# Kernel optimization log

Hardware: AMD Instinct MI355X
Metric: run time of the kernel (lower is better)

The kernel has to match this reference:

```python
import jax, jax.numpy as jnp
import numpy as np

B, T, D = 16, 512, 256          # batch, seq_len, d_model (= num features = num graph nodes N)
H, MC, K, DE, DH = 4, 4, 3, 10, 128
GS, SS, AS = 4, 6, 4            # global/sector/asset regime states
TAU = 0.5
STEPS = 3                       # diffusion steps
HID = max(64, D)
DEC_H = max(64, D // 2)


def setup_inputs() -> dict:
    key = jax.random.key(0)
    ks = iter(jax.random.split(key, 64))

    def nrm(shape, s=0.02):
        return (s * jax.random.normal(next(ks), shape)).astype(jnp.float32)

    z = lambda *s: jnp.zeros(s, jnp.float32)
    o = lambda *s: jnp.ones(s, jnp.float32)
    p = dict(
        x=jax.random.normal(next(ks), (B, T, D), dtype=jnp.float32),
        # hierarchical regime controller
        gW1=nrm((D, HID)), gb1=z(HID), g_ln_w=o(HID), g_ln_b=z(HID),
        gW2=nrm((HID, GS)), gb2=z(GS),
        sW1=nrm((D, HID)), sb1=z(HID), sW2=nrm((HID, D * SS)), sb2=z(D * SS),
        aW1=nrm((D, HID)), ab1=z(HID), aW2=nrm((HID, D * AS)), ab2=z(D * AS),
        global_prior=z(GS), sector_prior=z(SS), asset_prior=z(AS),
        g2f=nrm((GS, D)),
        sector_emb=jax.random.normal(next(ks), (SS, D), dtype=jnp.float32),
        asset_emb=jax.random.normal(next(ks), (AS, D), dtype=jnp.float32),
        # bidirectional temporal scan (BI-Mamba stand-in)
        decay_f=nrm((D,), 1.0), decay_b=nrm((D,), 1.0),
        tW=nrm((D, D)), tb=z(D),
        # Bayesian MAGAC + diffusion graph prior
        psi=nrm((H, D, DE), 0.1), log_sigma=jnp.full((H,), -2.0, jnp.float32),
        step_logits=jnp.linspace(-1.0, 0.5, STEPS).astype(jnp.float32),
        noise_scale=jnp.full((STEPS,), 0.05, jnp.float32),
        Wk=nrm((K + 1, T, DH)),
        mean_w=nrm((DH,)), mean_b=z(), lv_w=nrm((DH,)), lv_b=z(),
        # risk-aware decoder
        dW1=nrm((D, DEC_H)), db1=z(DEC_H), d_ln_w=o(DEC_H), d_ln_b=z(DEC_H),
        mW=nrm((DEC_H,)), mb=z(), lvW=nrm((DEC_H,)), lvb=z(),
        cW=nrm((DEC_H,)), cb=z(),
    )
    return p


def _ln(h, w, b):
    m = h.mean(-1, keepdims=True)
    v = h.var(-1, keepdims=True)  # biased, matches torch LayerNorm
    return (h - m) / jnp.sqrt(v + 1e-5) * w + b


def _gelu(h):
    return jax.nn.gelu(h, approximate=False)


def _gumbel_softmax(k, logits):
    u = jax.random.uniform(k, logits.shape, minval=1e-6, maxval=1.0 - 1e-6)
    g = -jnp.log(-jnp.log(u))
    return jax.nn.softmax((logits + g) / TAU, axis=-1)


def _fwd(x, gW1, gb1, g_ln_w, g_ln_b, gW2, gb2, sW1, sb1, sW2, sb2,
         aW1, ab1, aW2, ab2, global_prior, sector_prior, asset_prior,
         g2f, sector_emb, asset_emb, decay_f, decay_b, tW, tb,
         psi, log_sigma, step_logits, noise_scale, Wk,
         mean_w, mean_b, lv_w, lv_b,
         dW1, db1, d_ln_w, d_ln_b, mW, mb, lvW, lvb, cW, cb):
    rk = jax.random.key(42)
    k_g, k_s, k_a, k_eps, k_diff = jax.random.split(rk, 5)

    # ---- hierarchical regime controller ----
    seq_mean = x.mean(1)                               # (B, D)
    diff_summary = (x[:, 1:] - x[:, :-1]).mean(1)      # (B, D)
    g_logits = _gelu(_ln(seq_mean @ gW1 + gb1, g_ln_w, g_ln_b)) @ gW2 + gb2
    s_logits = (_gelu(seq_mean @ sW1 + sb1) @ sW2 + sb2).reshape(B, D, SS)
    a_logits = (_gelu(diff_summary @ aW1 + ab1) @ aW2 + ab2).reshape(B, D, AS)
    g_probs = _gumbel_softmax(k_g, g_logits)
    s_probs = _gumbel_softmax(k_s, s_logits)
    a_probs = _gumbel_softmax(k_a, a_logits)
    global_gate = g_probs @ g2f                                   # (B, D)
    # diagonal of einsum('bfs,sd->bfd') == einsum('bfs,sf->bf')
    sector_gate = jnp.einsum('bfs,sf->bf', s_probs, sector_emb)
    asset_gate = jnp.einsum('bfs,sf->bf', a_probs, asset_emb)
    feature_gate = jax.nn.sigmoid(global_gate + sector_gate + asset_gate)
    gated_x = x * feature_gate[:, None, :]

    # ---- bidirectional temporal EMA scan (BI-Mamba stand-in) ----
    af = jax.nn.sigmoid(decay_f)
    abk = jax.nn.sigmoid(decay_b)
    xs = gated_x.transpose(1, 0, 2)                    # (T, B, D)

    def ema(a):
        def step(h, xt):
            h = a * h + (1.0 - a) * xt
            return h, h
        return step

    _, hf = jax.lax.scan(ema(af), jnp.zeros_like(xs[0]), xs)
    _, hb = jax.lax.scan(ema(abk), jnp.zeros_like(xs[0]), xs[::-1])
    temporal = (hf + hb[::-1]).transpose(1, 0, 2) @ tW + tb       # (B, T, D)
    node_major = temporal.transpose(0, 2, 1)                      # (B, N=D, T)

    # ---- Bayesian adjacency sampling (MC samples per head) ----
    logits = jnp.einsum('hne,hme->hnm', psi, psi) / jnp.sqrt(jnp.float32(DE))
    sigma = jnp.exp(log_sigma)                                    # (H,)
    eps = jax.random.normal(k_eps, (MC, H, D, D))
    A = jax.nn.softmax(logits[None] + sigma[None, :, None, None] * eps, axis=-1)

    # ---- diffusion refinement guided by regime features ----
    ctx = feature_gate.mean(0)
    ctx = ctx / (jnp.linalg.norm(ctx) + 1e-6)
    outer = ctx[:, None] * ctx[None, :]
    outer = outer / jnp.maximum(outer.sum(-1, keepdims=True), 1e-6)
    dkeys = jax.random.split(k_diff, STEPS)
    for s in range(STEPS):                             # fixed small loop, vectorized over (MC,H)
        alpha = jax.nn.sigmoid(step_logits[s])
        noise = noise_scale[s] * jax.random.normal(dkeys[s], A.shape)
        A = alpha * A + (1.0 - alpha) * outer + noise
        A = 0.5 * (A + jnp.swapaxes(A, -1, -2))
        A = jax.nn.softmax(A, axis=-1)

    # ---- K-hop graph conv, averaged over MC samples and heads ----
    Z = jnp.einsum('bnt,td->bnd', node_major, Wk[0])[None, None]  # hop 0
    P = jnp.broadcast_to(node_major, (MC, H, B, D, T))
    for k in range(1, K + 1):
        P = jnp.einsum('mhnp,mhbpt->mhbnt', A, P)
        Z = Z + jnp.einsum('mhbnt,td->mhbnd', P, Wk[k])
    Z = Z.mean((0, 1))                                            # (B, N, DH)
    graph_mean = Z @ mean_w + mean_b                              # (B, N)
    graph_logvar = Z @ lv_w + lv_b                                # (B, N)

    # ---- risk-aware decoder ----
    feat = _ln(_gelu(graph_mean @ dW1 + db1), d_ln_w, d_ln_b)     # (B, DEC_H)
    mean = feat @ mW + mb
    dec_logvar = feat @ lvW + lvb
    _cvar = jax.nn.sigmoid(feat @ cW + cb)  # auxiliary head (not in returned output)
    var = jnp.exp(dec_logvar) + jnp.exp(graph_logvar).sum(1)
    log_var = jnp.log(var)
    return jnp.stack([mean, log_var], axis=-1)                    # (B, 2)


def reference(x, gW1, gb1, g_ln_w, g_ln_b, gW2, gb2, sW1, sb1, sW2, sb2,
              aW1, ab1, aW2, ab2, global_prior, sector_prior, asset_prior,
              g2f, sector_emb, asset_emb, decay_f, decay_b, tW, tb,
              psi, log_sigma, step_logits, noise_scale, Wk,
              mean_w, mean_b, lv_w, lv_b,
              dW1, db1, d_ln_w, d_ln_b, mW, mb, lvW, lvb, cW, cb):
    return _fwd(x, gW1, gb1, g_ln_w, g_ln_b, gW2, gb2, sW1, sb1, sW2, sb2,
                aW1, ab1, aW2, ab2, global_prior, sector_prior, asset_prior,
                g2f, sector_emb, asset_emb, decay_f, decay_b, tW, tb,
                psi, log_sigma, step_logits, noise_scale, Wk,
                mean_w, mean_b, lv_w, lv_b,
                dW1, db1, d_ln_w, d_ln_b, mW, mb, lvW, lvb, cW, cb)
```

## Files before the change

### kernel.cpp

```cpp
#include <hip/hip_runtime.h>
#include <stdint.h>

#define PARTITIONABLE 1

namespace {

struct TFPair { uint32_t a, b; };

__host__ __device__ constexpr uint32_t rotl32(uint32_t x, int d) {
  return (x << d) | (x >> (32 - d));
}

__host__ __device__ constexpr TFPair tf2x32(uint32_t k0, uint32_t k1,
                                            uint32_t x0, uint32_t x1) {
  uint32_t k2 = k0 ^ k1 ^ 0x1BD11BDAu;
  x0 += k0; x1 += k1;
  x0 += x1; x1 = rotl32(x1, 13); x1 ^= x0;
  x0 += x1; x1 = rotl32(x1, 15); x1 ^= x0;
  x0 += x1; x1 = rotl32(x1, 26); x1 ^= x0;
  x0 += x1; x1 = rotl32(x1, 6);  x1 ^= x0;
  x0 += k1; x1 += k2 + 1u;
  x0 += x1; x1 = rotl32(x1, 17); x1 ^= x0;
  x0 += x1; x1 = rotl32(x1, 29); x1 ^= x0;
  x0 += x1; x1 = rotl32(x1, 16); x1 ^= x0;
// ... 71 lines not shown
__device__ __forceinline__ float erfinv_f32(float x) {
  float w = -log1pf(-x * x);
  float p;
  if (w < 5.0f) {
    w -= 2.5f;
    p = 2.81022636e-08f;
    p = fmaf(p, w, 3.43273939e-07f);
    p = fmaf(p, w, -3.5233877e-06f);
    p = fmaf(p, w, -4.39150654e-06f);
    p = fmaf(p, w, 0.00021858087f);
    p = fmaf(p, w, -0.00125372503f);
    p = fmaf(p, w, -0.00417768164f);
    p = fmaf(p, w, 0.246640727f);
    p = fmaf(p, w, 1.50140941f);
  } else {
    w = sqrtf(w) - 3.0f;
    p = -0.000200214257f;
    p = fmaf(p, w, 0.000100950558f);
    p = fmaf(p, w, 0.00134934322f);
    p = fmaf(p, w, -0.00367342844f);
    p = fmaf(p, w, 0.00573950773f);
    p = fmaf(p, w, -0.0076224613f);
    p = fmaf(p, w, 0.00943887047f);
    p = fmaf(p, w, 1.00167406f);
    p = fmaf(p, w, 2.83297682f);
  }
  return p * x;
}

__device__ __forceinline__ float normal_from(uint32_t k0, uint32_t k1,
                                             uint32_t idx, uint32_t half) {
  const float lo = -0x1.fffffep-1f;
  float f = bits_to_u01(rbits(k0, k1, idx, half));
  float u = fmaxf(lo, f * 2.0f + lo);
  return 1.41421356237f * erfinv_f32(u);
}

__device__ __forceinline__ float gelu_f(float x) {
  return 0.5f * x * (1.0f + erff(x / 1.4142135623730951f));
}
__device__ __forceinline__ float sigmoid_f(float x) {
  return 1.0f / (1.0f + expf(-x));
}

__device__ __forceinline__ float wave_sum(float v) {
  #pragma unroll
  for (int m = 32; m > 0; m >>= 1) v += __shfl_xor(v, m);
  return v;
}
__device__ __forceinline__ float wave_max(float v) {
  #pragma unroll
  for (int m = 32; m > 0; m >>= 1) v = fmaxf(v, __shfl_xor(v, m));
  return v;
}
template <int NW>
__device__ __forceinline__ float blk_sum(float v, float* slots) {
  v = wave_sum(v);
  int wid = threadIdx.x >> 6;
  if ((threadIdx.x & 63) == 0) slots[wid] = v;
  __syncthreads();
  float r = slots[0];
  #pragma unroll
  for (int i = 1; i < NW; ++i) r += slots[i];
  return r;
}
template <int NW>
__device__ __forceinline__ float blk_max(float v, float* slots) {
  v = wave_max(v);
  int wid = threadIdx.x >> 6;
  if ((threadIdx.x & 63) == 0) slots[wid] = v;
  __syncthreads();
  float r = slots[0];
  #pragma unroll
  for (int i = 1; i < NW; ++i) r = fmaxf(r, slots[i]);
  return r;
}

struct Params {
  const float *x, *gW1, *gb1, *glnw, *glnb, *gW2, *gb2, *sW1, *sb1, *sW2, *sb2,
      *aW1, *ab1, *aW2, *ab2, *g2f, *semb, *aemb, *decay_f, *decay_b, *tW, *tb,
      *psi, *log_sigma, *step_logits, *noise_scale, *Wk, *mean_w, *mean_b,
      *lv_w, *lv_b, *dW1, *db1, *dlnw, *dlnb, *mW, *mb, *lvW, *lvb;
  float* out;
  float *ps, *ds, *fg, *ctx, *v, *sv, *u, *Pf, *Qf, *Pb, *Qb, *Lf, *Lb, *YH,
      *R1, *gm, *glv, *A, *A2, *At, *At2;
};


__device__ __forceinline__ void phase_ps(const Params& P, int bid, int tid) {
  int b = bid >> 4, tc = bid & 15;
  const float* xp = P.x + ((size_t)b * 512 + tc * 32) * 256 + tid;
  float s = 0.f;
  for (int i = 0; i < 32; ++i) s += xp[(size_t)i * 256];
  P.ps[(size_t)bid * 256 + tid] = s;
  if (tc == 0) {
    const float* xb = P.x + (size_t)b * 512 * 256 + tid;
    P.ds[b * 256 + tid] = (xb[(size_t)511 * 256] - xb[0]) / 511.0f;
  }
}

__device__ __forceinline__ void phase_hidgates(const Params& P, float* smem,
                                               int task, int tid) {
  float* seqm = smem;
  float* dif  = smem + 256;
  float* hgGs = smem + 512;
  float* hgSs = smem + 768;
  float* hgAs = smem + 1024;
  float* lvS  = smem + 1280;
  float* lvA  = smem + 1664;
  float* gsl  = smem + 1920;
  float* gvals= smem + 1936;
  float* gpv  = smem + 1940;
  float* s1   = smem + 1944;
  float* s2   = smem + 1948;
  int b = task >> 2, f0 = (task & 3) * 64;
  const float* psb = P.ps + (size_t)(b * 16) * 256 + tid;
  float s = 0.f;
  for (int tc = 0; tc < 16; ++tc) s += psb[(size_t)tc * 256];
  seqm[tid] = s / 512.0f;
  dif[tid] = P.ds[b * 256 + tid];
  __syncthreads();
  float hG = P.gb1[tid], hS = P.sb1[tid], hA = P.ab1[tid];
  for (int d = 0; d < 256; ++d) {
    float sm = seqm[d], df = dif[d];
    hG = fmaf(sm, P.gW1[d * 256 + tid], hG);
    hS = fmaf(sm, P.sW1[d * 256 + tid], hS);
    hA = fmaf(df, P.aW1[d * 256 + tid], hA);
  }
  {
    float mean = blk_sum<4>(hG, s1) / 256.0f;
    float dv = hG - mean;
    float var = blk_sum<4>(dv * dv, s2) / 256.0f;
    hG = dv / sqrtf(var + 1e-5f) * P.glnw[tid] + P.glnb[tid];
  }
  hgGs[tid] = gelu_f(hG);
  hgSs[tid] = gelu_f(hS);
  hgAs[tid] = gelu_f(hA);
  __syncthreads();
  float lg[4];
  #pragma unroll
  for (int sx = 0; sx < 4; ++sx)
    lg[sx] = blk_sum<4>(hgGs[tid] * P.gW2[tid * 4 + sx], gsl + 4 * sx);
  if (tid < 4) {
    float u = gumbel_u(KG.a, KG.b, (uint32_t)(b * 4 + tid), 32u);
    float g = -logf(-logf(u));
    gvals[tid] = (lg[tid] + P.gb2[tid] + g) / 0.5f;
  }
  __syncthreads();
  if (tid < 4) {
    float mx = fmaxf(fmaxf(gvals[0], gvals[1]), fmaxf(gvals[2], gvals[3]));
    float sum = expf(gvals[0] - mx) + expf(gvals[1] - mx) +
                expf(gvals[2] - mx) + expf(gvals[3] - mx);
    gpv[tid] = expf(gvals[tid] - mx) / sum;
  }
  {
    int o = tid;
    int fl = o / 6, sx = o - fl * 6;
    int f = f0 + fl;
    const float* wp = P.sW2 + f * 6 + sx;
    float acc = P.sb2[f * 6 + sx];
    for (int d = 0; d < 256; ++d) acc = fmaf(hgSs[d], wp[(size_t)d * 1536], acc);
    float u = gumbel_u(KS.a, KS.b, (uint32_t)(b * 256 + f) * 6u + sx, 12288u);
    lvS[o] = (acc + (-logf(-logf(u)))) / 0.5f;
  }
  if (tid < 128) {
    int o = tid + 256;
    int fl = o / 6, sx = o - fl * 6;
    int f = f0 + fl;
    const float* wp = P.sW2 + f * 6 + sx;
    float acc = P.sb2[f * 6 + sx];
    for (int d = 0; d < 256; ++d) acc = fmaf(hgSs[d], wp[(size_t)d * 1536], acc);
    float u = gumbel_u(KS.a, KS.b, (uint32_t)(b * 256 + f) * 6u + sx, 12288u);
    lvS[o] = (acc + (-logf(-logf(u)))) / 0.5f;
  }
  {
    int fl = tid >> 2, sx = tid & 3;
    int f = f0 + fl;
    const float* wp = P.aW2 + f * 4 + sx;
    float acc = P.ab2[f * 4 + sx];
    for (int d = 0; d < 256; ++d) acc = fmaf(hgAs[d], wp[(size_t)d * 1024], acc);
    float u = gumbel_u(KA.a, KA.b, (uint32_t)(b * 256 + f) * 4u + sx, 8192u);
    lvA[tid] = (acc + (-logf(-logf(u)))) / 0.5f;
  }
  __syncthreads();
  if (tid < 64) {
    int f = f0 + tid;
    float v0 = lvS[tid * 6 + 0], v1 = lvS[tid * 6 + 1], v2 = lvS[tid * 6 + 2];
    float v3 = lvS[tid * 6 + 3], v4 = lvS[tid * 6 + 4], v5 = lvS[tid * 6 + 5];
    float mx = fmaxf(fmaxf(fmaxf(v0, v1), fmaxf(v2, v3)), fmaxf(v4, v5));
    float e0 = expf(v0 - mx), e1 = expf(v1 - mx), e2 = expf(v2 - mx);
    float e3 = expf(v3 - mx), e4 = expf(v4 - mx), e5 = expf(v5 - mx);
    float ssum = e0 + e1 + e2 + e3 + e4 + e5;
    float sg = (e0 / ssum) * P.semb[0 * 256 + f] + (e1 / ssum) * P.semb[1 * 256 + f] +
               (e2 / ssum) * P.semb[2 * 256 + f] + (e3 / ssum) * P.semb[3 * 256 + f] +
               (e4 / ssum) * P.semb[4 * 256 + f] + (e5 / ssum) * P.semb[5 * 256 + f];
    float a0 = lvA[tid * 4 + 0], a1 = lvA[tid * 4 + 1];
    float a2 = lvA[tid * 4 + 2], a3 = lvA[tid * 4 + 3];
    float amx = fmaxf(fmaxf(a0, a1), fmaxf(a2, a3));
    float x0 = expf(a0 - amx), x1 = expf(a1 - amx);
    float x2 = expf(a2 - amx), x3 = expf(a3 - amx);
    float asum = x0 + x1 + x2 + x3;
    float ag = (x0 / asum) * P.aemb[0 * 256 + f] + (x1 / asum) * P.aemb[1 * 256 + f] +
               (x2 / asum) * P.aemb[2 * 256 + f] + (x3 / asum) * P.aemb[3 * 256 + f];
    float gg = 0.f;
    #pragma unroll
    for (int sx = 0; sx < 4; ++sx) gg = fmaf(gpv[sx], P.g2f[sx * 256 + f], gg);
    P.fg[b * 256 + f] = sigmoid_f(gg + sg + ag);
  }
}

__device__ __forceinline__ void phase_vcompute(const Params& P, int bid2,
                                               int tid) {
  int j = bid2 >> 2, tg = bid2 & 3;
  const float* wp = (j & 1) ? P.lv_w : P.mean_w;
  const float* Wkk = P.Wk + (size_t)(j >> 1) * 65536;
  int wid = tid >> 6, lane = tid & 63;
  float w0 = wp[lane], w1 = wp[64 + lane];
  float svloc = 0.f;
  for (int i = 0; i < 32; ++i) {
    int t = tg * 128 + wid * 32 + i;
    const float* row = Wkk + (size_t)t * 128;
    float s = row[lane] * w0 + row[64 + lane] * w1;
    s = wave_sum(s);
    if (lane == 0) { P.v[j * 512 + t] = s; svloc += s; }
  }
  if (lane == 0) P.sv[j * 16 + tg * 4 + wid] = svloc;
}

__device__ __forceinline__ void phase_ainit_row(const Params& P, float* smem,
                                                int blk, int tid) {
  float* pn = smem;
  float* s1 = smem + 12;
  float* s2 = smem + 16;
  int mh = blk >> 8, h = mh & 3, n = blk & 255, p = tid;
  if (p < 10) pn[p] = P.psi[(size_t)(h * 256 + n) * 10 + p];
  __syncthreads();
  const float* pp = P.psi + (size_t)(h * 256 + p) * 10;
  float s = 0.f;
  #pragma unroll
  for (int e = 0; e < 10; ++e) s = fmaf(pn[e], pp[e], s);
  float logit = s / sqrtf(10.0f);
  uint32_t idx = (uint32_t)blk * 256u + (uint32_t)p;
  float eps = normal_from(KE.a, KE.b, idx, 524288u);
  float val = logit + expf(P.log_sigma[h]) * eps;
  float mx = blk_max<4>(val, s1);
  float e = expf(val - mx);
  float sum = blk_sum<4>(e, s2);
  P.A[(size_t)blk * 256 + p] = e / sum;
}

__device__ __forceinline__ void phase_ctx(const Params& P, float* smem,
                                          int tid) {
  float* s1 = smem;
  float* s2 = smem + 4;
  float c = 0.f;
  for (int b = 0; b < 16; ++b) c += P.fg[b * 256 + tid];
  c /= 16.0f;
  float ss = blk_sum<4>(c * c, s1);
  float cv = c / (sqrtf(ss) + 1e-6f);
  P.ctx[tid] = cv;
  float S = blk_sum<4>(cv, s2);
  if (tid == 0) P.ctx[256] = S;
}

__device__ __forceinline__ void phase_transA(const Params& P, float* smem,
                                             int blk, int tid) {
  float* tile = smem;
  int mh = blk >> 6;
  int tr = ((blk >> 3) & 7) * 32, tc = (blk & 7) * 32;
  const float* src = P.A + (size_t)mh * 65536;
  float* dst = P.At + (size_t)mh * 65536;
  int lr = tid >> 5, lc = tid & 31;
  #pragma unroll
  for (int p = 0; p < 4; ++p) {
    int r = p * 8 + lr;
    tile[r * 33 + lc] = src[(size_t)(tr + r) * 256 + tc + lc];
  }
  __syncthreads();
  #pragma unroll
  for (int p = 0; p < 4; ++p) {
    int r = p * 8 + lr;
    dst[(size_t)(tc + r) * 256 + tr + lc] = tile[lc * 33 + r];
  }
}

__device__ __forceinline__ void phase_scan1(const Params& P, float* smem,
                                            int ch, int tid) {
  float* vv = smem;
  int b = ch >> 4, c = ch & 15;
  int d = tid;
  vv[(d >> 5) * 32 + (d & 31)] = P.v[(d >> 5) * 512 + c * 32 + (d & 31)];
// ... 127 lines not shown
                                           float* AoutT, uint32_t dk0,
                                           uint32_t dk1, int blk, int tid) {
  float* vals = smem;
  float* slots = smem + 4 * 257;
  int mh = blk >> 6, r0 = (blk & 63) * 4;
  float alpha = sigmoid_f(P.step_logits[sidx]);
  float ns = P.noise_scale[sidx];
  float S = P.ctx[256];
  int c = tid;
  float cp = P.ctx[c];
  const size_t mbase = (size_t)mh * 65536;
  #pragma unroll
  for (int r = 0; r < 4; ++r) {
    int n = r0 + r;
    float cn = P.ctx[n];
    float o_np = (cn * cp) / fmaxf(cn * S, 1e-6f);
    float o_pn = (cp * cn) / fmaxf(cp * S, 1e-6f);
    uint32_t i_np = (uint32_t)(mh * 65536 + n * 256 + c);
    uint32_t i_pn = (uint32_t)(mh * 65536 + c * 256 + n);
    float a_np = Ain[mbase + (size_t)n * 256 + c];
    float a_pn = AinT[mbase + (size_t)n * 256 + c];
    float m_np = alpha * a_np + (1.0f - alpha) * o_np +
                 ns * normal_from(dk0, dk1, i_np, 524288u);
    float m_pn = alpha * a_pn + (1.0f - alpha) * o_pn +
                 ns * normal_from(dk0, dk1, i_pn, 524288u);
    vals[r * 257 + c] = 0.5f * (m_np + m_pn);
  }
  __syncthreads();
  #pragma unroll
  for (int r = 0; r < 4; ++r) {
    float val = vals[r * 257 + c];
    float mx = blk_max<4>(val, slots + r * 8);
    float e = expf(val - mx);
    float sum = blk_sum<4>(e, slots + r * 8 + 4);
    float o = e / sum;
    Aout[mbase + (size_t)(r0 + r) * 256 + c] = o;
    if (WRITE_T) vals[r * 257 + c] = o;
  }
  if (WRITE_T) {
    __syncthreads();
    float t0 = vals[0 * 257 + c], t1 = vals[1 * 257 + c];
    float t2 = vals[2 * 257 + c], t3 = vals[3 * 257 + c];
    float4* dst = (float4*)(AoutT + mbase + (size_t)c * 256 + r0);
    dst[0] = make_float4(t0, t1, t2, t3);
  }
}

__device__ __forceinline__ void phase_findec(const Params& P, float* smem,
                                             int bid, int tid) {
  float* gmv = smem;
  float* sl = smem + 256;
  int b = bid;
  float sm_ = 0.f, sl_ = 0.f;
  for (int mh = 0; mh < 16; ++mh) {
    sm_ += P.R1[(size_t)mh * 8192 + tid * 32 + b * 2];
    sl_ += P.R1[(size_t)mh * 8192 + tid * 32 + b * 2 + 1];
  }
  float gmn = P.gm[b * 256 + tid] + sm_ * (1.0f / 16.0f);
  float gln = P.glv[b * 256 + tid] + sl_ * (1.0f / 16.0f);
  gmv[tid] = gmn;
  float se = expf(gln);
  __syncthreads();
  float sumexp = blk_sum<4>(se, sl);
  float h = 0.f;
  if (tid < 128) {
    h = P.db1[tid];
    for (int n = 0; n < 256; ++n) h = fmaf(gmv[n], P.dW1[n * 128 + tid], h);
    h = gelu_f(h);
  }
  float mean = blk_sum<4>(tid < 128 ? h : 0.f, sl + 4) / 128.0f;
  float dv = (tid < 128) ? h - mean : 0.f;
  float var = blk_sum<4>(dv * dv, sl + 8) / 128.0f;
  float feat = (tid < 128) ? dv / sqrtf(var + 1e-5f) * P.dlnw[tid] + P.dlnb[tid]
                           : 0.f;
  float m_c = blk_sum<4>(tid < 128 ? feat * P.mW[tid] : 0.f, sl + 12) + P.mb[0];
  float lv_c = blk_sum<4>(tid < 128 ? feat * P.lvW[tid] : 0.f, sl + 16) + P.lvb[0];
  if (tid == 0) {
    P.out[b * 2 + 0] = m_c;
    P.out[b * 2 + 1] = logf(expf(lv_c) + sumexp);
  }
}


__global__ __launch_bounds__(256) void kPre(Params P) {
  __shared__ float smem[20];
  int bid = blockIdx.x, tid = threadIdx.x;
  if (bid < 256) phase_ps(P, bid, tid);
  else if (bid < 288) phase_vcompute(P, bid - 256, tid);
  else phase_ainit_row(P, smem, bid - 288, tid);
}

__global__ __launch_bounds__(256) void kGate(Params P) {
  __shared__ float smem[1952];
  int bid = blockIdx.x, tid = threadIdx.x;
  if (bid < 64) phase_hidgates(P, smem, bid, tid);
  else phase_transA(P, smem, bid - 64, tid);
}

__global__ __launch_bounds__(256) void kScan(Params P) {
  __shared__ float smem[256];
  int bid = blockIdx.x, tid = threadIdx.x;
  if (bid < 256) phase_scan1(P, smem, bid, tid);
  else phase_ctx(P, smem, tid);
}

__global__ __launch_bounds__(256) void kM0(Params P) {
  __shared__ float smem[1060];
  int bid = blockIdx.x, tid = threadIdx.x;
  if (bid < 1024)
    phase_mix4<true>(P, smem, 0, P.A, P.At, P.A2, P.At2, DK0.a, DK0.b, bid, tid);
  else
    phase_scan2(P, bid - 1024, tid);
}

__global__ __launch_bounds__(256) void kM1(Params P) {
  __shared__ float smem[2120];
  int bid = blockIdx.x, tid = threadIdx.x;
  if (bid < 1024)
    phase_mix4<true>(P, smem, 1, P.A2, P.At2, P.A, P.At, DK1.a, DK1.b, bid, tid);
  else
    phase_ygemm(P, smem, bid - 1024, tid);
}

__global__ __launch_bounds__(256) void kM2(Params P) {
  __shared__ float smem[1060];
  phase_mix4<false>(P, smem, 2, P.A, P.At, P.A2, nullptr, DK2.a, DK2.b,
                    blockIdx.x, threadIdx.x);
}

__global__ __launch_bounds__(256) void kHor(Params P) {
  __shared__ float Rc[512];
  int bid = blockIdx.x, tid = threadIdx.x;
  int mh = bid >> 4, c0 = (bid & 15) * 2;
  const float* Ab = P.A2 + (size_t)mh * 65536;
  const float4* Arow = (const float4*)(Ab + (size_t)tid * 256);
  const float* Y2 = P.YH + 2 * 8192;
  Rc[tid * 2 + 0] = Y2[tid * 32 + c0 + 0];
  Rc[tid * 2 + 1] = Y2[tid * 32 + c0 + 1];
  __syncthreads();
  #pragma unroll
  for (int hop = 0; hop < 3; ++hop) {
    float acc0 = 0.f, acc1 = 0.f;
    const float4* Rc4 = (const float4*)Rc;
    for (int k4 = 0; k4 < 64; ++k4) {
      float4 a = Arow[k4];
      float4 r01 = Rc4[k4 * 2];
      float4 r23 = Rc4[k4 * 2 + 1];
      acc0 = fmaf(a.x, r01.x, acc0); acc1 = fmaf(a.x, r01.y, acc1);
      acc0 = fmaf(a.y, r01.z, acc0); acc1 = fmaf(a.y, r01.w, acc1);
      acc0 = fmaf(a.z, r23.x, acc0); acc1 = fmaf(a.z, r23.y, acc1);
      acc0 = fmaf(a.w, r23.z, acc0); acc1 = fmaf(a.w, r23.w, acc1);
    }
    if (hop == 0) {
      acc0 += P.YH[8192 + tid * 32 + c0 + 0];
      acc1 += P.YH[8192 + tid * 32 + c0 + 1];
    } else if (hop == 1) {
      acc0 += P.YH[tid * 32 + c0 + 0];
      acc1 += P.YH[tid * 32 + c0 + 1];
    }
    __syncthreads();
    Rc[tid * 2 + 0] = acc0;
    Rc[tid * 2 + 1] = acc1;
    __syncthreads();
  }
  P.R1[(size_t)mh * 8192 + (size_t)tid * 32 + c0 + 0] = Rc[tid * 2 + 0];
  P.R1[(size_t)mh * 8192 + (size_t)tid * 32 + c0 + 1] = Rc[tid * 2 + 1];
}

__global__ __launch_bounds__(256) void kFin(Params P) {
  __shared__ float smem[276];
  phase_findec(P, smem, blockIdx.x, threadIdx.x);
}

constexpr size_t O_FG = 0;
constexpr size_t O_CTX = 4096;
constexpr size_t O_V = 4480;
constexpr size_t O_SV = 8576;
constexpr size_t O_U = 8704;
constexpr size_t O_PF = 41472;
constexpr size_t O_QF = 565760;
constexpr size_t O_PB = 1090048;
constexpr size_t O_QB = 1614336;
constexpr size_t O_LF = 2138624;
constexpr size_t O_LB = 2204160;
constexpr size_t O_YH = 2269696;
constexpr size_t O_R1 = 2294272;
constexpr size_t O_GM = 2425344;
constexpr size_t O_GLV = 2429440;
constexpr size_t O_A = 2433536;
constexpr size_t O_A2 = 3482112;
constexpr size_t O_AT = 4530688;
constexpr size_t O_AT2 = 5579264;
constexpr size_t O_PS = 6627840;
constexpr size_t O_DS = 6693376;

}

extern "C" void kernel_launch(void* const* d_in, const int* in_sizes, int n_in,
                              void* d_out, int out_size, void* d_ws,
                              size_t ws_size, hipStream_t stream) {
  (void)in_sizes; (void)n_in; (void)out_size; (void)ws_size;
  float* w = (float*)d_ws;
  Params prm;
  prm.x = (const float*)d_in[0];
  prm.gW1 = (const float*)d_in[1];
  prm.gb1 = (const float*)d_in[2];
  prm.glnw = (const float*)d_in[3];
  prm.glnb = (const float*)d_in[4];
  prm.gW2 = (const float*)d_in[5];
  prm.gb2 = (const float*)d_in[6];
  prm.sW1 = (const float*)d_in[7];
  prm.sb1 = (const float*)d_in[8];
  prm.sW2 = (const float*)d_in[9];
  prm.sb2 = (const float*)d_in[10];
  prm.aW1 = (const float*)d_in[11];
  prm.ab1 = (const float*)d_in[12];
  prm.aW2 = (const float*)d_in[13];
  prm.ab2 = (const float*)d_in[14];
  prm.g2f = (const float*)d_in[18];
  prm.semb = (const float*)d_in[19];
  prm.aemb = (const float*)d_in[20];
  prm.decay_f = (const float*)d_in[21];
  prm.decay_b = (const float*)d_in[22];
  prm.tW = (const float*)d_in[23];
  prm.tb = (const float*)d_in[24];
  prm.psi = (const float*)d_in[25];
  prm.log_sigma = (const float*)d_in[26];
  prm.step_logits = (const float*)d_in[27];
  prm.noise_scale = (const float*)d_in[28];
  prm.Wk = (const float*)d_in[29];
  prm.mean_w = (const float*)d_in[30];
  prm.mean_b = (const float*)d_in[31];
  prm.lv_w = (const float*)d_in[32];
  prm.lv_b = (const float*)d_in[33];
  prm.dW1 = (const float*)d_in[34];
  prm.db1 = (const float*)d_in[35];
  prm.dlnw = (const float*)d_in[36];
  prm.dlnb = (const float*)d_in[37];
  prm.mW = (const float*)d_in[38];
  prm.mb = (const float*)d_in[39];
  prm.lvW = (const float*)d_in[40];
  prm.lvb = (const float*)d_in[41];
  prm.out = (float*)d_out;
  prm.fg = w + O_FG;
  prm.ctx = w + O_CTX;
  prm.v = w + O_V;
  prm.sv = w + O_SV;
  prm.u = w + O_U;
  prm.Pf = w + O_PF;
  prm.Qf = w + O_QF;
  prm.Pb = w + O_PB;
  prm.Qb = w + O_QB;
  prm.Lf = w + O_LF;
  prm.Lb = w + O_LB;
  prm.YH = w + O_YH;
  prm.R1 = w + O_R1;
  prm.gm = w + O_GM;
  prm.glv = w + O_GLV;
  prm.A = w + O_A;
  prm.A2 = w + O_A2;
  prm.At = w + O_AT;
  prm.At2 = w + O_AT2;
  prm.ps = w + O_PS;
  prm.ds = w + O_DS;

  kPre<<<4384, 256, 0, stream>>>(prm);
  kGate<<<1088, 256, 0, stream>>>(prm);
  kScan<<<257, 256, 0, stream>>>(prm);
  kM0<<<1152, 256, 0, stream>>>(prm);
  kM1<<<1056, 256, 0, stream>>>(prm);
  kM2<<<1024, 256, 0, stream>>>(prm);
  kHor<<<256, 256, 0, stream>>>(prm);
  kFin<<<16, 256, 0, stream>>>(prm);
}
```

Measured before the change: 310.9 us.

## Compute regime gates with one block per batch instead of four

The hidden-layer/gate phase used four blocks per batch, each recomputing the same 256-wide hidden layers. It now uses one block per batch. The first-layer matvec is split across three heads using float4 weight loads. Each thread then owns one feature and computes all six sector and four asset logits in registers, with vectorised asset-weight loads. This removes redundant first-layer work and the shared-memory staging of logits, but each gate block now does more serial work, with fewer blocks in flight alongside the transA blocks.

After: 364.7 us. 1.17x slower.

```diff
diff --git a/kernel.cpp b/kernel.cpp
--- a/kernel.cpp
+++ b/kernel.cpp
@@ -194,48 +194,69 @@
   }
 }
 
-__device__ __forceinline__ void phase_hidgates(const Params& P, float* smem,
-                                               int task, int tid) {
+__device__ __forceinline__ void phase_hidgates16(const Params& P, float* smem,
+                                                 int b, int tid) {
   float* seqm = smem;
   float* dif  = smem + 256;
-  float* hgGs = smem + 512;
-  float* hgSs = smem + 768;
-  float* hgAs = smem + 1024;
-  float* lvS  = smem + 1280;
-  float* lvA  = smem + 1664;
-  float* gsl  = smem + 1920;
-  float* gvals= smem + 1936;
-  float* gpv  = smem + 1940;
-  float* s1   = smem + 1944;
-  float* s2   = smem + 1948;
-  int b = task >> 2, f0 = (task & 3) * 64;
+  float* rawG = smem + 512;
+  float* rawS = smem + 768;
+  float* rawA = smem + 1024;
+  float* gsl  = smem + 1280;
+  float* gvals= smem + 1296;
+  float* gpv  = smem + 1300;
+  float* s1   = smem + 1304;
+  float* s2   = smem + 1308;
   const float* psb = P.ps + (size_t)(b * 16) * 256 + tid;
   float s = 0.f;
   for (int tc = 0; tc < 16; ++tc) s += psb[(size_t)tc * 256];
   seqm[tid] = s / 512.0f;
   dif[tid] = P.ds[b * 256 + tid];
   __syncthreads();
-  float hG = P.gb1[tid], hS = P.sb1[tid], hA = P.ab1[tid];
-  for (int d = 0; d < 256; ++d) {
-    float sm = seqm[d], df = dif[d];
-    hG = fmaf(sm, P.gW1[d * 256 + tid], hG);
-    hS = fmaf(sm, P.sW1[d * 256 + tid], hS);
-    hA = fmaf(df, P.aW1[d * 256 + tid], hA);
-  }
+  if (tid < 192) {
+    int head = tid >> 6;
+    int o4 = (tid & 63) * 4;
+    const float* W = (head == 0) ? P.gW1 : (head == 1) ? P.sW1 : P.aW1;
+    const float* bias = (head == 0) ? P.gb1 : (head == 1) ? P.sb1 : P.ab1;
+    const float* src = (head == 2) ? dif : seqm;
+    float4 acc = *(const float4*)(bias + o4);
+    for (int d0 = 0; d0 < 256; d0 += 8) {
+      float4 wv[8];
+      #pragma unroll
+      for (int q = 0; q < 8; ++q)
+        wv[q] = *(const float4*)(W + (size_t)(d0 + q) * 256 + o4);
+      #pragma unroll
+      for (int q = 0; q < 8; ++q) {
+        float sv = src[d0 + q];
+        acc.x = fmaf(sv, wv[q].x, acc.x);
+        acc.y = fmaf(sv, wv[q].y, acc.y);
+        acc.z = fmaf(sv, wv[q].z, acc.z);
+        acc.w = fmaf(sv, wv[q].w, acc.w);
+      }
+    }
+    float* dst = (head == 0) ? rawG : (head == 1) ? rawS : rawA;
+    dst[o4 + 0] = acc.x;
+    dst[o4 + 1] = acc.y;
+    dst[o4 + 2] = acc.z;
+    dst[o4 + 3] = acc.w;
+  }
+  __syncthreads();
   {
+    float hG = rawG[tid];
     float mean = blk_sum<4>(hG, s1) / 256.0f;
     float dv = hG - mean;
     float var = blk_sum<4>(dv * dv, s2) / 256.0f;
     hG = dv / sqrtf(var + 1e-5f) * P.glnw[tid] + P.glnb[tid];
-  }
-  hgGs[tid] = gelu_f(hG);
-  hgSs[tid] = gelu_f(hS);
-  hgAs[tid] = gelu_f(hA);
+    float hS = rawS[tid];
+    float hA = rawA[tid];
+    rawG[tid] = gelu_f(hG);
+    rawS[tid] = gelu_f(hS);
+    rawA[tid] = gelu_f(hA);
+  }
   __syncthreads();
   float lg[4];
   #pragma unroll
   for (int sx = 0; sx < 4; ++sx)
-    lg[sx] = blk_sum<4>(hgGs[tid] * P.gW2[tid * 4 + sx], gsl + 4 * sx);
+    lg[sx] = blk_sum<4>(rawG[tid] * P.gW2[tid * 4 + sx], gsl + 4 * sx);
   if (tid < 4) {
     float u = gumbel_u(KG.a, KG.b, (uint32_t)(b * 4 + tid), 32u);
     float g = -logf(-logf(u));
@@ -248,60 +269,65 @@
                 expf(gvals[2] - mx) + expf(gvals[3] - mx);
     gpv[tid] = expf(gvals[tid] - mx) / sum;
   }
+  int f = tid;
+  float sacc[6];
+  #pragma unroll
+  for (int sx = 0; sx < 6; ++sx) sacc[sx] = P.sb2[f * 6 + sx];
+  float4 aacc = *(const float4*)(P.ab2 + f * 4);
+  const float* swp = P.sW2 + f * 6;
+  const float* awp = P.aW2 + f * 4;
+  for (int d0 = 0; d0 < 256; d0 += 4) {
+    #pragma unroll
+    for (int q = 0; q < 4; ++q) {
+      int d = d0 + q;
+      float hs = rawS[d], ha = rawA[d];
+      #pragma unroll
+      for (int sx = 0; sx < 6; ++sx)
+        sacc[sx] = fmaf(hs, swp[(size_t)d * 1536 + sx], sacc[sx]);
+      float4 a4 = *(const float4*)(awp + (size_t)d * 1024);
+      aacc.x = fmaf(ha, a4.x, aacc.x);
+      aacc.y = fmaf(ha, a4.y, aacc.y);
+      aacc.z = fmaf(ha, a4.z, aacc.z);
+      aacc.w = fmaf(ha, a4.w, aacc.w);
+    }
+  }
+  float vv[6];
+  #pragma unroll
+  for (int sx = 0; sx < 6; ++sx) {
+    float u = gumbel_u(KS.a, KS.b, (uint32_t)(b * 256 + f) * 6u + sx, 12288u);
+    vv[sx] = (sacc[sx] + (-logf(-logf(u)))) / 0.5f;
+  }
+  float aa[4];
   {
-    int o = tid;
-    int fl = o / 6, sx = o - fl * 6;
-    int f = f0 + fl;
-    const float* wp = P.sW2 + f * 6 + sx;
-    float acc = P.sb2[f * 6 + sx];
-    for (int d = 0; d < 256; ++d) acc = fmaf(hgSs[d], wp[(size_t)d * 1536], acc);
-    float u = gumbel_u(KS.a, KS.b, (uint32_t)(b * 256 + f) * 6u + sx, 12288u);
-    lvS[o] = (acc + (-logf(-logf(u)))) / 0.5f;
-  }
-  if (tid < 128) {
-    int o = tid + 256;
-    int fl = o / 6, sx = o - fl * 6;
-    int f = f0 + fl;
-    const float* wp = P.sW2 + f * 6 + sx;
-    float acc = P.sb2[f * 6 + sx];
-    for (int d = 0; d < 256; ++d) acc = fmaf(hgSs[d], wp[(size_t)d * 1536], acc);
-    float u = gumbel_u(KS.a, KS.b, (uint32_t)(b * 256 + f) * 6u + sx, 12288u);
-    lvS[o] = (acc + (-logf(-logf(u)))) / 0.5f;
-  }
-  {
-    int fl = tid >> 2, sx = tid & 3;
-    int f = f0 + fl;
-    const float* wp = P.aW2 + f * 4 + sx;
-    float acc = P.ab2[f * 4 + sx];
-    for (int d = 0; d < 256; ++d) acc = fmaf(hgAs[d], wp[(size_t)d * 1024], acc);
-    float u = gumbel_u(KA.a, KA.b, (uint32_t)(b * 256 + f) * 4u + sx, 8192u);
-    lvA[tid] = (acc + (-logf(-logf(u)))) / 0.5f;
-  }
-  __syncthreads();
-  if (tid < 64) {
-    int f = f0 + tid;
-    float v0 = lvS[tid * 6 + 0], v1 = lvS[tid * 6 + 1], v2 = lvS[tid * 6 + 2];
-    float v3 = lvS[tid * 6 + 3], v4 = lvS[tid * 6 + 4], v5 = lvS[tid * 6 + 5];
-    float mx = fmaxf(fmaxf(fmaxf(v0, v1), fmaxf(v2, v3)), fmaxf(v4, v5));
-    float e0 = expf(v0 - mx), e1 = expf(v1 - mx), e2 = expf(v2 - mx);
-    float e3 = expf(v3 - mx), e4 = expf(v4 - mx), e5 = expf(v5 - mx);
-    float ssum = e0 + e1 + e2 + e3 + e4 + e5;
-    float sg = (e0 / ssum) * P.semb[0 * 256 + f] + (e1 / ssum) * P.semb[1 * 256 + f] +
-               (e2 / ssum) * P.semb[2 * 256 + f] + (e3 / ssum) * P.semb[3 * 256 + f] +
-               (e4 / ssum) * P.semb[4 * 256 + f] + (e5 / ssum) * P.semb[5 * 256 + f];
-    float a0 = lvA[tid * 4 + 0], a1 = lvA[tid * 4 + 1];
-    float a2 = lvA[tid * 4 + 2], a3 = lvA[tid * 4 + 3];
-    float amx = fmaxf(fmaxf(a0, a1), fmaxf(a2, a3));
-    float x0 = expf(a0 - amx), x1 = expf(a1 - amx);
-    float x2 = expf(a2 - amx), x3 = expf(a3 - amx);
-    float asum = x0 + x1 + x2 + x3;
-    float ag = (x0 / asum) * P.aemb[0 * 256 + f] + (x1 / asum) * P.aemb[1 * 256 + f] +
-               (x2 / asum) * P.aemb[2 * 256 + f] + (x3 / asum) * P.aemb[3 * 256 + f];
-    float gg = 0.f;
-    #pragma unroll
-    for (int sx = 0; sx < 4; ++sx) gg = fmaf(gpv[sx], P.g2f[sx * 256 + f], gg);
-    P.fg[b * 256 + f] = sigmoid_f(gg + sg + ag);
-  }
+    float u0 = gumbel_u(KA.a, KA.b, (uint32_t)(b * 256 + f) * 4u + 0, 8192u);
+    float u1 = gumbel_u(KA.a, KA.b, (uint32_t)(b * 256 + f) * 4u + 1, 8192u);
+    float u2 = gumbel_u(KA.a, KA.b, (uint32_t)(b * 256 + f) * 4u + 2, 8192u);
+    float u3 = gumbel_u(KA.a, KA.b, (uint32_t)(b * 256 + f) * 4u + 3, 8192u);
+    aa[0] = (aacc.x + (-logf(-logf(u0)))) / 0.5f;
+    aa[1] = (aacc.y + (-logf(-logf(u1)))) / 0.5f;
+    aa[2] = (aacc.z + (-logf(-logf(u2)))) / 0.5f;
+    aa[3] = (aacc.w + (-logf(-logf(u3)))) / 0.5f;
+  }
+  __syncthreads();
+  float v0 = vv[0], v1 = vv[1], v2 = vv[2], v3 = vv[3], v4 = vv[4], v5 = vv[5];
+  float mx = fmaxf(fmaxf(fmaxf(v0, v1), fmaxf(v2, v3)), fmaxf(v4, v5));
+  float e0 = expf(v0 - mx), e1 = expf(v1 - mx), e2 = expf(v2 - mx);
+  float e3 = expf(v3 - mx), e4 = expf(v4 - mx), e5 = expf(v5 - mx);
+  float ssum = e0 + e1 + e2 + e3 + e4 + e5;
+  float sg = (e0 / ssum) * P.semb[0 * 256 + f] + (e1 / ssum) * P.semb[1 * 256 + f] +
+             (e2 / ssum) * P.semb[2 * 256 + f] + (e3 / ssum) * P.semb[3 * 256 + f] +
+             (e4 / ssum) * P.semb[4 * 256 + f] + (e5 / ssum) * P.semb[5 * 256 + f];
+  float a0 = aa[0], a1 = aa[1], a2 = aa[2], a3 = aa[3];
+  float amx = fmaxf(fmaxf(a0, a1), fmaxf(a2, a3));
+  float x0 = expf(a0 - amx), x1 = expf(a1 - amx);
+  float x2 = expf(a2 - amx), x3 = expf(a3 - amx);
+  float asum = x0 + x1 + x2 + x3;
+  float ag = (x0 / asum) * P.aemb[0 * 256 + f] + (x1 / asum) * P.aemb[1 * 256 + f] +
+             (x2 / asum) * P.aemb[2 * 256 + f] + (x3 / asum) * P.aemb[3 * 256 + f];
+  float gg = 0.f;
+  #pragma unroll
+  for (int sx = 0; sx < 4; ++sx) gg = fmaf(gpv[sx], P.g2f[sx * 256 + f], gg);
+  P.fg[b * 256 + f] = sigmoid_f(gg + sg + ag);
 }
 
 __device__ __forceinline__ void phase_vcompute(const Params& P, int bid2,
@@ -604,10 +630,10 @@
 }
 
 __global__ __launch_bounds__(256) void kGate(Params P) {
-  __shared__ float smem[1952];
+  __shared__ float smem[1312];
   int bid = blockIdx.x, tid = threadIdx.x;
-  if (bid < 64) phase_hidgates(P, smem, bid, tid);
-  else phase_transA(P, smem, bid - 64, tid);
+  if (bid < 16) phase_hidgates16(P, smem, bid, tid);
+  else phase_transA(P, smem, bid - 16, tid);
 }
 
 __global__ __launch_bounds__(256) void kScan(Params P) {
@@ -778,7 +804,7 @@
   prm.ds = w + O_DS;
 
   kPre<<<4384, 256, 0, stream>>>(prm);
-  kGate<<<1088, 256, 0, stream>>>(prm);
+  kGate<<<1040, 256, 0, stream>>>(prm);
   kScan<<<257, 256, 0, stream>>>(prm);
   kM0<<<1152, 256, 0, stream>>>(prm);
   kM1<<<1056, 256, 0, stream>>>(prm);
```

## Split regime-gate MLP into per-head and column-tiled GEMM stages

Applied to the files above, without the earlier changes.

Replaces the partial-sum pass and the monolithic 64-block gate kernel with three stages. The first computes each head's first layer per batch: 48 blocks, with each mean block reducing x over time itself. The second runs the sector and asset second-layer GEMMs across 160 column-tiled blocks, and the third does the softmax/embedding gate combine. The aim is to stop every gate block recomputing all three first-layer matvecs and to spread the large sW2/aW2 reads over more blocks. In exchange it adds a kernel launch, global-memory round trips for intermediates, and 32 redundant full-sequence reads of x in the first stage.

Result: faster. 294.6 us (median of 3 runs) (-5.2%).

```diff
diff --git a/kernel.cpp b/kernel.cpp
--- a/kernel.cpp
+++ b/kernel.cpp
@@ -177,65 +177,49 @@
       *psi, *log_sigma, *step_logits, *noise_scale, *Wk, *mean_w, *mean_b,
       *lv_w, *lv_b, *dW1, *db1, *dlnw, *dlnb, *mW, *mb, *lvW, *lvb;
   float* out;
-  float *ps, *ds, *fg, *ctx, *v, *sv, *u, *Pf, *Qf, *Pb, *Qb, *Lf, *Lb, *YH,
-      *R1, *gm, *glv, *A, *A2, *At, *At2;
+  float *fg, *ctx, *v, *sv, *u, *Pf, *Qf, *Pb, *Qb, *Lf, *Lb, *YH,
+      *R1, *gm, *glv, *A, *A2, *At, *At2, *hgS, *hgA, *lvS, *lvA, *gpv;
 };
 
 
-__device__ __forceinline__ void phase_ps(const Params& P, int bid, int tid) {
-  int b = bid >> 4, tc = bid & 15;
-  const float* xp = P.x + ((size_t)b * 512 + tc * 32) * 256 + tid;
-  float s = 0.f;
-  for (int i = 0; i < 32; ++i) s += xp[(size_t)i * 256];
-  P.ps[(size_t)bid * 256 + tid] = s;
-  if (tc == 0) {
-    const float* xb = P.x + (size_t)b * 512 * 256 + tid;
-    P.ds[b * 256 + tid] = (xb[(size_t)511 * 256] - xb[0]) / 511.0f;
-  }
-}
-
-__device__ __forceinline__ void phase_hidgates(const Params& P, float* smem,
-                                               int task, int tid) {
-  float* seqm = smem;
-  float* dif  = smem + 256;
-  float* hgGs = smem + 512;
-  float* hgSs = smem + 768;
-  float* hgAs = smem + 1024;
-  float* lvS  = smem + 1280;
-  float* lvA  = smem + 1664;
-  float* gsl  = smem + 1920;
-  float* gvals= smem + 1936;
-  float* gpv  = smem + 1940;
-  float* s1   = smem + 1944;
-  float* s2   = smem + 1948;
-  int b = task >> 2, f0 = (task & 3) * 64;
-  const float* psb = P.ps + (size_t)(b * 16) * 256 + tid;
-  float s = 0.f;
-  for (int tc = 0; tc < 16; ++tc) s += psb[(size_t)tc * 256];
-  seqm[tid] = s / 512.0f;
-  dif[tid] = P.ds[b * 256 + tid];
-  __syncthreads();
-  float hG = P.gb1[tid], hS = P.sb1[tid], hA = P.ab1[tid];
-  for (int d = 0; d < 256; ++d) {
-    float sm = seqm[d], df = dif[d];
-    hG = fmaf(sm, P.gW1[d * 256 + tid], hG);
-    hS = fmaf(sm, P.sW1[d * 256 + tid], hS);
-    hA = fmaf(df, P.aW1[d * 256 + tid], hA);
-  }
-  {
-    float mean = blk_sum<4>(hG, s1) / 256.0f;
-    float dv = hG - mean;
-    float var = blk_sum<4>(dv * dv, s2) / 256.0f;
-    hG = dv / sqrtf(var + 1e-5f) * P.glnw[tid] + P.glnb[tid];
-  }
-  hgGs[tid] = gelu_f(hG);
-  hgSs[tid] = gelu_f(hS);
-  hgAs[tid] = gelu_f(hA);
-  __syncthreads();
+__device__ __forceinline__ void phase_w1head(const Params& P, float* smem,
+                                             int blk, int tid) {
+  float* src  = smem;
+  float* s1   = smem + 256;
+  float* s2   = smem + 260;
+  float* gsl  = smem + 264;
+  float* gvals= smem + 280;
+  int head = blk >> 4, b = blk & 15;
+  const float* xb = P.x + (size_t)b * 512 * 256 + tid;
+  if (head < 2) {
+    float s = 0.f;
+    for (int tc = 0; tc < 16; ++tc) {
+      float ps = 0.f;
+      #pragma unroll
+      for (int i = 0; i < 32; ++i) ps += xb[(size_t)(tc * 32 + i) * 256];
+      s += ps;
+    }
+    src[tid] = s / 512.0f;
+  } else {
+    src[tid] = (xb[(size_t)511 * 256] - xb[0]) / 511.0f;
+  }
+  __syncthreads();
+  const float* W = (head == 0) ? P.gW1 : (head == 1) ? P.sW1 : P.aW1;
+  const float* bias = (head == 0) ? P.gb1 : (head == 1) ? P.sb1 : P.ab1;
+  float acc = bias[tid];
+  #pragma unroll 8
+  for (int d = 0; d < 256; ++d)
+    acc = fmaf(src[d], W[(size_t)d * 256 + tid], acc);
+  if (head == 1) { P.hgS[b * 256 + tid] = gelu_f(acc); return; }
+  if (head == 2) { P.hgA[b * 256 + tid] = gelu_f(acc); return; }
+  float mean = blk_sum<4>(acc, s1) / 256.0f;
+  float dv = acc - mean;
+  float var = blk_sum<4>(dv * dv, s2) / 256.0f;
+  float hg = gelu_f(dv / sqrtf(var + 1e-5f) * P.glnw[tid] + P.glnb[tid]);
   float lg[4];
   #pragma unroll
   for (int sx = 0; sx < 4; ++sx)
-    lg[sx] = blk_sum<4>(hgGs[tid] * P.gW2[tid * 4 + sx], gsl + 4 * sx);
+    lg[sx] = blk_sum<4>(hg * P.gW2[tid * 4 + sx], gsl + 4 * sx);
   if (tid < 4) {
     float u = gumbel_u(KG.a, KG.b, (uint32_t)(b * 4 + tid), 32u);
     float g = -logf(-logf(u));
@@ -246,62 +230,65 @@
     float mx = fmaxf(fmaxf(gvals[0], gvals[1]), fmaxf(gvals[2], gvals[3]));
     float sum = expf(gvals[0] - mx) + expf(gvals[1] - mx) +
                 expf(gvals[2] - mx) + expf(gvals[3] - mx);
-    gpv[tid] = expf(gvals[tid] - mx) / sum;
-  }
-  {
-    int o = tid;
-    int fl = o / 6, sx = o - fl * 6;
-    int f = f0 + fl;
-    const float* wp = P.sW2 + f * 6 + sx;
-    float acc = P.sb2[f * 6 + sx];
-    for (int d = 0; d < 256; ++d) acc = fmaf(hgSs[d], wp[(size_t)d * 1536], acc);
+    P.gpv[b * 4 + tid] = expf(gvals[tid] - mx) / sum;
+  }
+}
+
+__device__ __forceinline__ void phase_l2gemm(const Params& P, float* smem,
+                                             int blk, int tid) {
+  float* h = smem;
+  if (blk < 96) {
+    int b = blk / 6, ct = blk % 6;
+    h[tid] = P.hgS[b * 256 + tid];
+    __syncthreads();
+    int col = ct * 256 + tid;
+    float acc = P.sb2[col];
+    const float* wp = P.sW2 + col;
+    #pragma unroll 8
+    for (int d = 0; d < 256; ++d) acc = fmaf(h[d], wp[(size_t)d * 1536], acc);
+    int f = col / 6, sx = col - f * 6;
     float u = gumbel_u(KS.a, KS.b, (uint32_t)(b * 256 + f) * 6u + sx, 12288u);
-    lvS[o] = (acc + (-logf(-logf(u)))) / 0.5f;
-  }
-  if (tid < 128) {
-    int o = tid + 256;
-    int fl = o / 6, sx = o - fl * 6;
-    int f = f0 + fl;
-    const float* wp = P.sW2 + f * 6 + sx;
-    float acc = P.sb2[f * 6 + sx];
-    for (int d = 0; d < 256; ++d) acc = fmaf(hgSs[d], wp[(size_t)d * 1536], acc);
-    float u = gumbel_u(KS.a, KS.b, (uint32_t)(b * 256 + f) * 6u + sx, 12288u);
-    lvS[o] = (acc + (-logf(-logf(u)))) / 0.5f;
-  }
-  {
-    int fl = tid >> 2, sx = tid & 3;
-    int f = f0 + fl;
-    const float* wp = P.aW2 + f * 4 + sx;
-    float acc = P.ab2[f * 4 + sx];
-    for (int d = 0; d < 256; ++d) acc = fmaf(hgAs[d], wp[(size_t)d * 1024], acc);
+    P.lvS[b * 1536 + col] = (acc + (-logf(-logf(u)))) / 0.5f;
+  } else {
+    int idx = blk - 96;
+    int b = idx >> 2, ct = idx & 3;
+    h[tid] = P.hgA[b * 256 + tid];
+    __syncthreads();
+    int col = ct * 256 + tid;
+    float acc = P.ab2[col];
+    const float* wp = P.aW2 + col;
+    #pragma unroll 8
+    for (int d = 0; d < 256; ++d) acc = fmaf(h[d], wp[(size_t)d * 1024], acc);
+    int f = col >> 2, sx = col & 3;
     float u = gumbel_u(KA.a, KA.b, (uint32_t)(b * 256 + f) * 4u + sx, 8192u);
-    lvA[tid] = (acc + (-logf(-logf(u)))) / 0.5f;
-  }
-  __syncthreads();
-  if (tid < 64) {
-    int f = f0 + tid;
-    float v0 = lvS[tid * 6 + 0], v1 = lvS[tid * 6 + 1], v2 = lvS[tid * 6 + 2];
-    float v3 = lvS[tid * 6 + 3], v4 = lvS[tid * 6 + 4], v5 = lvS[tid * 6 + 5];
-    float mx = fmaxf(fmaxf(fmaxf(v0, v1), fmaxf(v2, v3)), fmaxf(v4, v5));
-    float e0 = expf(v0 - mx), e1 = expf(v1 - mx), e2 = expf(v2 - mx);
-    float e3 = expf(v3 - mx), e4 = expf(v4 - mx), e5 = expf(v5 - mx);
-    float ssum = e0 + e1 + e2 + e3 + e4 + e5;
-    float sg = (e0 / ssum) * P.semb[0 * 256 + f] + (e1 / ssum) * P.semb[1 * 256 + f] +
-               (e2 / ssum) * P.semb[2 * 256 + f] + (e3 / ssum) * P.semb[3 * 256 + f] +
-               (e4 / ssum) * P.semb[4 * 256 + f] + (e5 / ssum) * P.semb[5 * 256 + f];
-    float a0 = lvA[tid * 4 + 0], a1 = lvA[tid * 4 + 1];
-    float a2 = lvA[tid * 4 + 2], a3 = lvA[tid * 4 + 3];
-    float amx = fmaxf(fmaxf(a0, a1), fmaxf(a2, a3));
-    float x0 = expf(a0 - amx), x1 = expf(a1 - amx);
-    float x2 = expf(a2 - amx), x3 = expf(a3 - amx);
-    float asum = x0 + x1 + x2 + x3;
-    float ag = (x0 / asum) * P.aemb[0 * 256 + f] + (x1 / asum) * P.aemb[1 * 256 + f] +
-               (x2 / asum) * P.aemb[2 * 256 + f] + (x3 / asum) * P.aemb[3 * 256 + f];
-    float gg = 0.f;
-    #pragma unroll
-    for (int sx = 0; sx < 4; ++sx) gg = fmaf(gpv[sx], P.g2f[sx * 256 + f], gg);
-    P.fg[b * 256 + f] = sigmoid_f(gg + sg + ag);
-  }
+    P.lvA[b * 1024 + col] = (acc + (-logf(-logf(u)))) / 0.5f;
+  }
+}
+
+__device__ __forceinline__ void phase_gfin(const Params& P, int b, int tid) {
+  int f = tid;
+  const float* lvSb = P.lvS + b * 1536 + f * 6;
+  float v0 = lvSb[0], v1 = lvSb[1], v2 = lvSb[2];
+  float v3 = lvSb[3], v4 = lvSb[4], v5 = lvSb[5];
+  float mx = fmaxf(fmaxf(fmaxf(v0, v1), fmaxf(v2, v3)), fmaxf(v4, v5));
+  float e0 = expf(v0 - mx), e1 = expf(v1 - mx), e2 = expf(v2 - mx);
+  float e3 = expf(v3 - mx), e4 = expf(v4 - mx), e5 = expf(v5 - mx);
+  float ssum = e0 + e1 + e2 + e3 + e4 + e5;
+  float sg = (e0 / ssum) * P.semb[0 * 256 + f] + (e1 / ssum) * P.semb[1 * 256 + f] +
+             (e2 / ssum) * P.semb[2 * 256 + f] + (e3 / ssum) * P.semb[3 * 256 + f] +
+             (e4 / ssum) * P.semb[4 * 256 + f] + (e5 / ssum) * P.semb[5 * 256 + f];
+  const float* lvAb = P.lvA + b * 1024 + f * 4;
+  float a0 = lvAb[0], a1 = lvAb[1], a2 = lvAb[2], a3 = lvAb[3];
+  float amx = fmaxf(fmaxf(a0, a1), fmaxf(a2, a3));
+  float x0 = expf(a0 - amx), x1 = expf(a1 - amx);
+  float x2 = expf(a2 - amx), x3 = expf(a3 - amx);
+  float asum = x0 + x1 + x2 + x3;
+  float ag = (x0 / asum) * P.aemb[0 * 256 + f] + (x1 / asum) * P.aemb[1 * 256 + f] +
+             (x2 / asum) * P.aemb[2 * 256 + f] + (x3 / asum) * P.aemb[3 * 256 + f];
+  float gg = 0.f;
+  #pragma unroll
+  for (int sx = 0; sx < 4; ++sx) gg = fmaf(P.gpv[b * 4 + sx], P.g2f[sx * 256 + f], gg);
+  P.fg[b * 256 + f] = sigmoid_f(gg + sg + ag);
 }
 
 __device__ __forceinline__ void phase_vcompute(const Params& P, int bid2,
@@ -595,19 +582,26 @@
 }
 
 
-__global__ __launch_bounds__(256) void kPre(Params P) {
-  __shared__ float smem[20];
+__global__ __launch_bounds__(256) void kA(Params P) {
+  __shared__ float smem[288];
   int bid = blockIdx.x, tid = threadIdx.x;
-  if (bid < 256) phase_ps(P, bid, tid);
-  else if (bid < 288) phase_vcompute(P, bid - 256, tid);
-  else phase_ainit_row(P, smem, bid - 288, tid);
-}
-
-__global__ __launch_bounds__(256) void kGate(Params P) {
-  __shared__ float smem[1952];
+  if (bid < 48) phase_w1head(P, smem, bid, tid);
+  else if (bid < 80) phase_vcompute(P, bid - 48, tid);
+  else phase_ainit_row(P, smem, bid - 80, tid);
+}
+
+__global__ __launch_bounds__(256) void kL2(Params P) {
+  __shared__ float smem[1056];
   int bid = blockIdx.x, tid = threadIdx.x;
-  if (bid < 64) phase_hidgates(P, smem, bid, tid);
-  else phase_transA(P, smem, bid - 64, tid);
+  if (bid < 160) phase_l2gemm(P, smem, bid, tid);
+  else phase_transA(P, smem, bid - 160, tid);
+}
+
+__global__ __launch_bounds__(256) void kGF(Params P) {
+  __shared__ float smem[1056];
+  int bid = blockIdx.x, tid = threadIdx.x;
+  if (bid < 16) phase_gfin(P, bid, tid);
+  else phase_transA(P, smem, bid - 16 + 512, tid);
 }
 
 __global__ __launch_bounds__(256) void kScan(Params P) {
@@ -704,8 +698,11 @@
 constexpr size_t O_A2 = 3482112;
 constexpr size_t O_AT = 4530688;
 constexpr size_t O_AT2 = 5579264;
-constexpr size_t O_PS = 6627840;
-constexpr size_t O_DS = 6693376;
+constexpr size_t O_HGS = 6627840;
+constexpr size_t O_HGA = 6631936;
+constexpr size_t O_LVS = 6636032;
+constexpr size_t O_LVA = 6660608;
+constexpr size_t O_GPV = 6676992;
 
 }
 
@@ -774,11 +771,15 @@
   prm.A2 = w + O_A2;
   prm.At = w + O_AT;
   prm.At2 = w + O_AT2;
-  prm.ps = w + O_PS;
-  prm.ds = w + O_DS;
-
-  kPre<<<4384, 256, 0, stream>>>(prm);
-  kGate<<<1088, 256, 0, stream>>>(prm);
+  prm.hgS = w + O_HGS;
+  prm.hgA = w + O_HGA;
+  prm.lvS = w + O_LVS;
+  prm.lvA = w + O_LVA;
+  prm.gpv = w + O_GPV;
+
+  kA<<<4176, 256, 0, stream>>>(prm);
+  kL2<<<672, 256, 0, stream>>>(prm);
+  kGF<<<528, 256, 0, stream>>>(prm);
   kScan<<<257, 256, 0, stream>>>(prm);
   kM0<<<1152, 256, 0, stream>>>(prm);
   kM1<<<1056, 256, 0, stream>>>(prm);
```
